# Optimization experiments

Hardware: AMD Instinct MI355X
Metric: run time of the kernel (lower is better)

## Reference

```python
import jax, jax.numpy as jnp
import numpy as np

DIM = 512
HEADS = 8
HEAD_DIM = 64
RS = 16        # region_size
EPEG_K = 15
L_TOKENS = 36864  # 192^2, multiple of RS^2 grid


def setup_inputs() -> dict:
    key = jax.random.key(0)
    ks = jax.random.split(key, 5)
    s = 1.0 / np.sqrt(DIM)
    x = jax.random.normal(ks[0], (1, L_TOKENS, DIM), jnp.float32)
    W_qkv = jax.random.normal(ks[1], (3 * HEADS * HEAD_DIM, DIM), jnp.float32) * s
    b_qkv = jnp.zeros((3 * HEADS * HEAD_DIM,), jnp.float32)
    W_proj = jax.random.normal(ks[2], (DIM, HEADS * HEAD_DIM), jnp.float32) * s
    b_proj = jnp.zeros((DIM,), jnp.float32)
    pe_w = jax.random.normal(ks[3], (HEADS, 1, EPEG_K, 1), jnp.float32) * 0.05
    pe_b = jnp.zeros((HEADS,), jnp.float32)
    return dict(x=x, W_qkv=W_qkv, b_qkv=b_qkv, W_proj=W_proj, b_proj=b_proj,
                pe_w=pe_w, pe_b=pe_b)


def reference(x, W_qkv, b_qkv, W_proj, b_proj, pe_w, pe_b):
    B, L, C = x.shape
    # --- padding() logic: square to HxW, H multiple of region_size ---
    H = int(np.ceil(np.sqrt(L)))
    H += (-H) % RS
    W = H
    add = H * W - L
    if add > 0:
        x = jnp.concatenate([x, jnp.zeros((B, add, C), x.dtype)], axis=1)
    # --- region_partition: (B,H,W,C) -> (num_regions*B, RS*RS, C) ---
    xr = (x.reshape(B, H // RS, RS, W // RS, RS, C)
            .transpose(0, 1, 3, 2, 4, 5)
            .reshape(-1, RS * RS, C))
    B_, N, _ = xr.shape
    # --- InnerAttention ---
    qkv = xr @ W_qkv.T + b_qkv                       # (B_, N, 3*h*d)
    qkv = qkv.reshape(B_, N, 3, HEADS, HEAD_DIM).transpose(2, 0, 3, 1, 4)
    q, k, v = qkv[0], qkv[1], qkv[2]                 # each (B_, h, N, d)
    scale = HEAD_DIM ** -0.5
    attn = jnp.einsum('bhid,bhjd->bhij', q * scale, k)   # (B_, h, N, N)
    # EPEG: depthwise conv (k,1) over the query axis of the score map
    pad = EPEG_K // 2
    pe = jax.lax.conv_general_dilated(
        attn, pe_w, window_strides=(1, 1), padding=((pad, pad), (0, 0)),
        dimension_numbers=('NCHW', 'OIHW', 'NCHW'), feature_group_count=HEADS)
    pe = pe + pe_b[None, :, None, None]
    attn = jax.nn.softmax(attn + pe, axis=-1)
    out = jnp.einsum('bhij,bhjd->bhid', attn, v)     # (B_, h, N, d)
    out = out.transpose(0, 2, 1, 3).reshape(B_, N, HEADS * HEAD_DIM)
    out = out @ W_proj.T + b_proj                    # (B_, N, C)
    # --- region_reverse ---
    out = (out.reshape(B, H // RS, W // RS, RS, RS, C)
              .transpose(0, 1, 3, 2, 4, 5)
              .reshape(B, H * W, C))
    if add > 0:
        out = out[:, :L]
    return out
```

## Files before the change

### kernel.cpp

```cpp
#include <hip/hip_runtime.h>
#include <stdint.h>

typedef __attribute__((ext_vector_type(8))) __bf16 bf16x8;
typedef __attribute__((ext_vector_type(16))) float f32x16;

__device__ __forceinline__ unsigned short f2bf(float f) {
  union { float f; unsigned int u; } v;
  v.f = f;
  unsigned int u = v.u;
  return (unsigned short)((u + 0x7FFFu + ((u >> 16) & 1u)) >> 16);
}

union BFrag { unsigned short u[8]; unsigned int w[4]; bf16x8 v; };

__device__ __forceinline__ f32x16 mfma32(bf16x8 a, bf16x8 b, f32x16 c) {
  return __builtin_amdgcn_mfma_f32_32x32x16_bf16(a, b, c, 0, 0, 0);
}

#define GLOAD_LDS16(gptr, lptr)                                                \
  __builtin_amdgcn_global_load_lds(                                           \
      (const __attribute__((address_space(1))) void*)(gptr),                  \
      (__attribute__((address_space(3))) void*)(lptr), 16, 0, 0)

__global__ __launch_bounds__(256) void k_xgather(const float* __restrict__ x,
                                                 unsigned short* __restrict__ xb) {
  int idx = blockIdx.x * 256 + threadIdx.x;
  int m = idx >> 6;
  int seg = (idx & 63) << 3;
  int r = m >> 8, n = m & 255;
  int a = r / 12, b = r - a * 12;
  int ii = n >> 4, jj = n & 15;
  long g = (long)((a * 16 + ii) * 192 + b * 16 + jj);
  const float4* p = (const float4*)(x + g * 512 + seg);
  float4 v0 = p[0], v1 = p[1];
  union { unsigned short u[8]; int4 v; } o;
  o.u[0] = f2bf(v0.x); o.u[1] = f2bf(v0.y); o.u[2] = f2bf(v0.z); o.u[3] = f2bf(v0.w);
  o.u[4] = f2bf(v1.x); o.u[5] = f2bf(v1.y); o.u[6] = f2bf(v1.z); o.u[7] = f2bf(v1.w);
  *(int4*)(xb + (size_t)m * 512 + seg) = o.v;
}

__global__ __launch_bounds__(256) void k_cvt(const float* __restrict__ s,
                                             unsigned short* __restrict__ d, int n8) {
  int i = blockIdx.x * 256 + threadIdx.x;
  if (i >= n8) return;
  const float4* p = (const float4*)(s + (size_t)i * 8);
  float4 a = p[0], b = p[1];
  union { unsigned short u[8]; int4 v; } o;
  o.u[0] = f2bf(a.x); o.u[1] = f2bf(a.y); o.u[2] = f2bf(a.z); o.u[3] = f2bf(a.w);
  o.u[4] = f2bf(b.x); o.u[5] = f2bf(b.y); o.u[6] = f2bf(b.z); o.u[7] = f2bf(b.w);
  *(int4*)(d + (size_t)i * 8) = o.v;
}

template<int MODE, int NBN>
__global__ __launch_bounds__(256, 2) void k_gemm(
    const unsigned short* __restrict__ A, const unsigned short* __restrict__ B,
    const float* __restrict__ bias,
    unsigned short* __restrict__ qb, unsigned short* __restrict__ kb,
    unsigned short* __restrict__ vtb, float* __restrict__ out) {
  __shared__ unsigned short As[8192];
  __shared__ unsigned short Bs[8192];
  int t = threadIdx.x;
  constexpr int NWG = NBN * 288;
  int d0 = blockIdx.x;
  int tl = (d0 & 7) * (NWG >> 3) + (d0 >> 3);
  int bm = tl / NBN, bn = tl % NBN;

  int w = t >> 6, lane = t & 63;
  int l31 = lane & 31, lh = lane >> 5;
  int wr = w >> 1, wc = w & 1;

  int srow = t >> 3, cseg = t & 7;
  int csw = (cseg ^ (srow & 7)) << 3;
  int ldsWaveOff = (t >> 6) << 10;

  f32x16 acc[2][2];
  for (int i = 0; i < 2; ++i)
    for (int j = 0; j < 2; ++j)
      for (int e = 0; e < 16; ++e) acc[i][j][e] = 0.0f;

  const unsigned short* Ag = A + (size_t)(bm * 128 + srow) * 512 + csw;
  const unsigned short* Bg = B + (size_t)(bn * 128 + srow) * 512 + csw;

  for (int ks = 0; ks < 8; ++ks) {
#pragma unroll
    for (int rnd = 0; rnd < 4; ++rnd) {
      GLOAD_LDS16(Ag + (size_t)rnd * 32 * 512 + ks * 64,
                  (char*)As + ldsWaveOff + rnd * 4096);
      GLOAD_LDS16(Bg + (size_t)rnd * 32 * 512 + ks * 64,
                  (char*)Bs + ldsWaveOff + rnd * 4096);
    }
    __syncthreads();
#pragma unroll
    for (int kt = 0; kt < 4; ++kt) {
      bf16x8 af[2], bfr[2];
#pragma unroll
      for (int mt = 0; mt < 2; ++mt) {
        int r = wr * 64 + mt * 32 + l31;
        af[mt] = *(const bf16x8*)((const char*)As + r * 128 +
                                  ((kt * 32 + lh * 16) ^ ((r & 7) << 4)));
      }
#pragma unroll
      for (int nt = 0; nt < 2; ++nt) {
        int r = wc * 64 + nt * 32 + l31;
        bfr[nt] = *(const bf16x8*)((const char*)Bs + r * 128 +
                                   ((kt * 32 + lh * 16) ^ ((r & 7) << 4)));
      }
#pragma unroll
      for (int mt = 0; mt < 2; ++mt)
#pragma unroll
        for (int nt = 0; nt < 2; ++nt)
          acc[mt][nt] = mfma32(af[mt], bfr[nt], acc[mt][nt]);
    }
    __syncthreads();
  }

  int nBase = bn * 128 + wc * 64;
  int mBase = bm * 128 + wr * 64;
#pragma unroll
  for (int nt = 0; nt < 2; ++nt) {
    int nn = nBase + nt * 32 + l31;
    float bs = bias[nn];
    if (MODE == 0) {
      int tsel = nn >> 9, rem = nn & 511;
      int hh = rem >> 6, d = rem & 63;
#pragma unroll
      for (int mt = 0; mt < 2; ++mt) {
#pragma unroll
        for (int q = 0; q < 4; ++q) {
          int m0 = mBase + mt * 32 + q * 8 + lh * 4;
          int r = m0 >> 8, tok = m0 & 255;
          size_t base = (size_t)(r * 8 + hh) * 16384;
          if (tsel == 0) {
#pragma unroll
            for (int j = 0; j < 4; ++j)
              qb[base + (size_t)(tok + j) * 64 + d] = f2bf((acc[mt][nt][q * 4 + j] + bs) * 0.125f);
          } else if (tsel == 1) {
#pragma unroll
            for (int j = 0; j < 4; ++j)
              kb[base + (size_t)(tok + j) * 64 + d] = f2bf(acc[mt][nt][q * 4 + j] + bs);
          } else {
            unsigned long long pv = 0;
#pragma unroll
            for (int j = 0; j < 4; ++j)
              pv |= (unsigned long long)f2bf(acc[mt][nt][q * 4 + j] + bs) << (16 * j);
            *(unsigned long long*)(vtb + base + (size_t)d * 256 + tok) = pv;
          }
        }
      }
    } else {
#pragma unroll
      for (int mt = 0; mt < 2; ++mt) {
#pragma unroll
        for (int q = 0; q < 4; ++q) {
          int m0 = mBase + mt * 32 + q * 8 + lh * 4;
          int r = m0 >> 8;
          int a = r / 12, bcol = r - a * 12;
#pragma unroll
          for (int j = 0; j < 4; ++j) {
            int tok = (m0 & 255) + j;
            int ii = tok >> 4, jj = tok & 15;
            long gg = (long)((a * 16 + ii) * 192 + bcol * 16 + jj);
            out[gg * 512 + nn] = acc[mt][nt][q * 4 + j] + bs;
          }
        }
      }
    }
  }
}

__global__ __launch_bounds__(512, 4) void k_attn6(
    const unsigned short* __restrict__ qb, const unsigned short* __restrict__ kb,
    const unsigned short* __restrict__ vtb, const float* __restrict__ pe_w,
    unsigned short* __restrict__ ctxb) {
  extern __shared__ char lds[];
  int rh = blockIdx.x;
  int h = rh & 7;
  int t = threadIdx.x, w = t >> 6, lane = t & 63;
  int l31 = lane & 31, lh = lane >> 5;
  int iw = w << 5;
  int myi = iw + l31;

  const unsigned short* Qg = qb + (size_t)rh * 16384;
  const unsigned short* Kg = kb + (size_t)rh * 16384;
  const unsigned short* Vg = vtb + (size_t)rh * 16384;
  const float* wh = pe_w + h * 15;

#pragma unroll
  for (int rr = 0; rr < 4; ++rr) {
    int row = rr * 64 + (t >> 3);
    GLOAD_LDS16(Kg + row * 64 + (((t & 7) ^ (row & 7)) << 3), lds + rr * 8192 + t * 16);
  }
  if (t < 96) {
    int dlo = t - 40, dhi = t - 39;
    unsigned int lo = (dlo >= 0 && dlo < 15) ? f2bf(wh[dlo]) : 0;
    unsigned int hi = (dhi >= 0 && dhi < 15) ? f2bf(wh[dhi]) : 0;
    *(unsigned int*)(lds + 57344 + t * 4) = lo | (hi << 16);
  }
  bf16x8 qf[4];
#pragma unroll
  for (int kt = 0; kt < 4; ++kt)
    qf[kt] = *(const bf16x8*)(Qg + (size_t)myi * 64 + kt * 16 + lh * 8);
  __syncthreads();

  float m = -3.0e38f, l = 0.0f;
  f32x16 acco[2];
#pragma unroll
  for (int nt = 0; nt < 2; ++nt)
#pragma unroll
    for (int e = 0; e < 16; ++e) acco[nt][e] = 0.0f;

#pragma unroll
  for (int it = 0; it < 8; ++it) {
    f32x16 sacc;
#pragma unroll
    for (int e = 0; e < 16; ++e) sacc[e] = 0.0f;
    {
      int kr = it * 32 + l31;
#pragma unroll
      for (int kt = 0; kt < 4; ++kt) {
        bf16x8 kf = *(const bf16x8*)(lds + kr * 128 + (((kt * 2 + lh) ^ (kr & 7)) << 4));
        sacc = mfma32(kf, qf[kt], sacc);
      }
    }
    __syncthreads();

    if ((it & 1) == 0) {
      int row = t >> 3;
      GLOAD_LDS16(Vg + row * 256 + it * 32 + (((t & 7) ^ (row & 7)) << 3),
                  lds + 49152 + t * 16);
    }

    {
      int i2 = myi * 2;
#pragma unroll
      for (int rg = 0; rg < 16; ++rg) {
        int jl = (rg & 3) + 8 * (rg >> 2) + 4 * lh;
        *(unsigned short*)(lds + 32768 + jl * 512 + (i2 ^ ((jl & 7) << 4))) =
            f2bf(sacc[rg]);
      }
    }
    __syncthreads();

    {
      int jl = l31;
#pragma unroll
      for (int u = 0; u < 4; ++u) {
        int ktg = 2 * w + u - 1;
        if (ktg >= 0 && ktg < 16) {
          BFrag bb;
          int d0 = 16 * u + 8 * lh - l31 + 31;
#pragma unroll
          for (int e2 = 0; e2 < 4; ++e2)
            bb.w[e2] = *(const unsigned int*)(lds + 57344 + (d0 + 2 * e2) * 4);
          bf16x8 sfr = *(const bf16x8*)(lds + 32768 + jl * 512 +
                                        ((ktg * 32 + lh * 16) ^ ((jl & 7) << 4)));
          sacc = mfma32(sfr, bb.v, sacc);
        }
      }
    }

    unsigned int pk[8];
    {
      float pm = -3.0e38f;
#pragma unroll
      for (int e = 0; e < 16; ++e) pm = fmaxf(pm, sacc[e]);
      pm = fmaxf(pm, __shfl_xor(pm, 32));
      float mn = fmaxf(m, pm);
      float f = __expf(m - mn);
      float ts = 0.0f;
#pragma unroll
      for (int u = 0; u < 8; ++u) {
        float p0 = __expf(sacc[2 * u] - mn);
        float p1 = __expf(sacc[2 * u + 1] - mn);
        ts += p0;
        ts += p1;
        pk[u] = (unsigned int)f2bf(p0) | ((unsigned int)f2bf(p1) << 16);
      }
      ts += __shfl_xor(ts, 32);
      l = (it == 0) ? ts : l * f + ts;
      m = mn;
      if (it != 0) {
#pragma unroll
        for (int rg = 0; rg < 16; ++rg) {
          float g = __shfl(f, (rg & 3) + 8 * (rg >> 2) + 4 * lh);
          acco[0][rg] *= g;
          acco[1][rg] *= g;
        }
      }
    }

    {
      unsigned int sw[8];
#pragma unroll
      for (int u = 0; u < 8; ++u) sw[u] = (unsigned int)__shfl_xor((int)pk[u], 32);
      BFrag pf0, pf1;
      if (lh == 0) {
        pf0.w[0] = pk[0]; pf0.w[1] = pk[1]; pf0.w[2] = sw[0]; pf0.w[3] = sw[1];
        pf1.w[0] = pk[4]; pf1.w[1] = pk[5]; pf1.w[2] = sw[4]; pf1.w[3] = sw[5];
      } else {
        pf0.w[0] = sw[2]; pf0.w[1] = sw[3]; pf0.w[2] = pk[2]; pf0.w[3] = pk[3];
        pf1.w[0] = sw[6]; pf1.w[1] = sw[7]; pf1.w[2] = pk[6]; pf1.w[3] = pk[7];
      }
      int kj0 = (it & 1) * 2;
#pragma unroll
      for (int nt = 0; nt < 2; ++nt) {
        int vr = nt * 32 + l31;
        bf16x8 vf0 = *(const bf16x8*)(lds + 49152 + vr * 128 +
                                      (((kj0 * 2 + lh) ^ (vr & 7)) << 4));
        bf16x8 vf1 = *(const bf16x8*)(lds + 49152 + vr * 128 +
                                      ((((kj0 + 1) * 2 + lh) ^ (vr & 7)) << 4));
        acco[nt] = mfma32(pf0.v, vf0, acco[nt]);
        acco[nt] = mfma32(pf1.v, vf1, acco[nt]);
      }
    }
  }

  float inv = 1.0f / l;
  int r256 = (rh >> 3) * 256;
  int chbase = h * 64;
#pragma unroll
  for (int rg = 0; rg < 16; ++rg) {
    int cr = (rg & 3) + 8 * (rg >> 2) + 4 * lh;
    float g = __shfl(inv, cr);
    int i = iw + cr;
    size_t rowoff = (size_t)(r256 + i) * 512 + chbase;
    ctxb[rowoff + l31] = f2bf(acco[0][rg] * g);
    ctxb[rowoff + 32 + l31] = f2bf(acco[1][rg] * g);
  }
}

extern "C" void kernel_launch(void* const* d_in, const int* in_sizes, int n_in,
                              void* d_out, int out_size, void* d_ws, size_t ws_size,
                              hipStream_t stream) {
  const float* x = (const float*)d_in[0];
  const float* Wqkv = (const float*)d_in[1];
  const float* bqkv = (const float*)d_in[2];
  const float* Wproj = (const float*)d_in[3];
  const float* bproj = (const float*)d_in[4];
  const float* pew = (const float*)d_in[5];

  char* ws = (char*)d_ws;
  unsigned short* xb = (unsigned short*)ws;
  unsigned short* wqkvb = (unsigned short*)(ws + 37748736);
  unsigned short* wprojb = (unsigned short*)(ws + 39321600);
  unsigned short* qb = (unsigned short*)(ws + 39845888);
  unsigned short* kb = (unsigned short*)(ws + 77594624);
  unsigned short* vtb = (unsigned short*)(ws + 115343360);

  (void)hipFuncSetAttribute((const void*)k_attn6,
                            hipFuncAttributeMaxDynamicSharedMemorySize, 163840);

  k_xgather<<<9216, 256, 0, stream>>>(x, xb);
  k_cvt<<<384, 256, 0, stream>>>(Wqkv, wqkvb, 98304);
  k_cvt<<<128, 256, 0, stream>>>(Wproj, wprojb, 32768);
  k_gemm<0, 12><<<3456, 256, 0, stream>>>(xb, wqkvb, bqkv, qb, kb, vtb, nullptr);
  k_attn6<<<1152, 512, 57728, stream>>>(qb, kb, vtb, pew, xb);
  k_gemm<1, 4><<<1152, 256, 0, stream>>>(xb, wprojb, bproj, nullptr, nullptr, nullptr,
                                         (float*)d_out);
}
```

Measured before the change: 244.7 us.

## Software-pipeline attention: double-buffer score tiles and V tiles, one barrier per step

Restructures the attention loop so the QK^T scores for the next key block are computed and staged into a second LDS buffer while the current block runs through the EPEG conv, softmax and PV. V tiles are also double-buffered and prefetched one step ahead, which cuts the loop from two barriers per iteration to one. The cost is more LDS (about 82KB per block, up from about 58KB) and extra accumulator registers. Launch bounds are relaxed from 4 to 2 blocks per SM, which lowers occupancy.

```diff
diff --git a/kernel.cpp b/kernel.cpp
--- a/kernel.cpp
+++ b/kernel.cpp
@@ -168,7 +168,7 @@
   }
 }
 
-__global__ __launch_bounds__(512, 4) void k_attn6(
+__global__ __launch_bounds__(512, 2) void k_attn7(
     const unsigned short* __restrict__ qb, const unsigned short* __restrict__ kb,
     const unsigned short* __restrict__ vtb, const float* __restrict__ pe_w,
     unsigned short* __restrict__ ctxb) {
@@ -190,11 +190,15 @@
     int row = rr * 64 + (t >> 3);
     GLOAD_LDS16(Kg + row * 64 + (((t & 7) ^ (row & 7)) << 3), lds + rr * 8192 + t * 16);
   }
+  {
+    int row = t >> 3;
+    GLOAD_LDS16(Vg + row * 256 + (((t & 7) ^ (row & 7)) << 3), lds + 65536 + t * 16);
+  }
   if (t < 96) {
     int dlo = t - 40, dhi = t - 39;
     unsigned int lo = (dlo >= 0 && dlo < 15) ? f2bf(wh[dlo]) : 0;
     unsigned int hi = (dhi >= 0 && dhi < 15) ? f2bf(wh[dhi]) : 0;
-    *(unsigned int*)(lds + 57344 + t * 4) = lo | (hi << 16);
+    *(unsigned int*)(lds + 81920 + t * 4) = lo | (hi << 16);
   }
   bf16x8 qf[4];
 #pragma unroll
@@ -209,37 +213,35 @@
 #pragma unroll
     for (int e = 0; e < 16; ++e) acco[nt][e] = 0.0f;
 
+  f32x16 sc[2];
+
+#pragma unroll
+  for (int e = 0; e < 16; ++e) sc[0][e] = 0.0f;
+  {
+    int kr = l31;
+#pragma unroll
+    for (int kt = 0; kt < 4; ++kt) {
+      bf16x8 kf = *(const bf16x8*)(lds + kr * 128 + (((kt * 2 + lh) ^ (kr & 7)) << 4));
+      sc[0] = mfma32(kf, qf[kt], sc[0]);
+    }
+  }
+  {
+    int i2 = myi * 2;
+#pragma unroll
+    for (int rg = 0; rg < 16; ++rg) {
+      int jl = (rg & 3) + 8 * (rg >> 2) + 4 * lh;
+      *(unsigned short*)(lds + 32768 + jl * 512 + (i2 ^ ((jl & 7) << 4))) =
+          f2bf(sc[0][rg]);
+    }
+  }
+  __syncthreads();
+
 #pragma unroll
   for (int it = 0; it < 8; ++it) {
-    f32x16 sacc;
-#pragma unroll
-    for (int e = 0; e < 16; ++e) sacc[e] = 0.0f;
-    {
-      int kr = it * 32 + l31;
-#pragma unroll
-      for (int kt = 0; kt < 4; ++kt) {
-        bf16x8 kf = *(const bf16x8*)(lds + kr * 128 + (((kt * 2 + lh) ^ (kr & 7)) << 4));
-        sacc = mfma32(kf, qf[kt], sacc);
-      }
-    }
-    __syncthreads();
-
-    if ((it & 1) == 0) {
-      int row = t >> 3;
-      GLOAD_LDS16(Vg + row * 256 + it * 32 + (((t & 7) ^ (row & 7)) << 3),
-                  lds + 49152 + t * 16);
-    }
-
-    {
-      int i2 = myi * 2;
-#pragma unroll
-      for (int rg = 0; rg < 16; ++rg) {
-        int jl = (rg & 3) + 8 * (rg >> 2) + 4 * lh;
-        *(unsigned short*)(lds + 32768 + jl * 512 + (i2 ^ ((jl & 7) << 4))) =
-            f2bf(sacc[rg]);
-      }
-    }
-    __syncthreads();
+    const int cur = it & 1, nxt = cur ^ 1;
+    char* sbuf = lds + 32768 + cur * 16384;
+    char* sbufN = lds + 32768 + nxt * 16384;
+    char* vbuf = lds + 65536 + ((it >> 1) & 1) * 8192;
 
     {
       int jl = l31;
@@ -251,11 +253,22 @@
           int d0 = 16 * u + 8 * lh - l31 + 31;
 #pragma unroll
           for (int e2 = 0; e2 < 4; ++e2)
-            bb.w[e2] = *(const unsigned int*)(lds + 57344 + (d0 + 2 * e2) * 4);
-          bf16x8 sfr = *(const bf16x8*)(lds + 32768 + jl * 512 +
+            bb.w[e2] = *(const unsigned int*)(lds + 81920 + (d0 + 2 * e2) * 4);
+          bf16x8 sfr = *(const bf16x8*)(sbuf + jl * 512 +
                                         ((ktg * 32 + lh * 16) ^ ((jl & 7) << 4)));
-          sacc = mfma32(sfr, bb.v, sacc);
+          sc[cur] = mfma32(sfr, bb.v, sc[cur]);
         }
+      }
+    }
+
+    if (it < 7) {
+#pragma unroll
+      for (int e = 0; e < 16; ++e) sc[nxt][e] = 0.0f;
+      int kr = (it + 1) * 32 + l31;
+#pragma unroll
+      for (int kt = 0; kt < 4; ++kt) {
+        bf16x8 kf = *(const bf16x8*)(lds + kr * 128 + (((kt * 2 + lh) ^ (kr & 7)) << 4));
+        sc[nxt] = mfma32(kf, qf[kt], sc[nxt]);
       }
     }
 
@@ -263,15 +276,15 @@
     {
       float pm = -3.0e38f;
 #pragma unroll
-      for (int e = 0; e < 16; ++e) pm = fmaxf(pm, sacc[e]);
+      for (int e = 0; e < 16; ++e) pm = fmaxf(pm, sc[cur][e]);
       pm = fmaxf(pm, __shfl_xor(pm, 32));
       float mn = fmaxf(m, pm);
       float f = __expf(m - mn);
       float ts = 0.0f;
 #pragma unroll
       for (int u = 0; u < 8; ++u) {
-        float p0 = __expf(sacc[2 * u] - mn);
-        float p1 = __expf(sacc[2 * u + 1] - mn);
+        float p0 = __expf(sc[cur][2 * u] - mn);
+        float p1 = __expf(sc[cur][2 * u + 1] - mn);
         ts += p0;
         ts += p1;
         pk[u] = (unsigned int)f2bf(p0) | ((unsigned int)f2bf(p1) << 16);
@@ -287,6 +300,23 @@
           acco[1][rg] *= g;
         }
       }
+    }
+
+    if (it < 7) {
+      int i2 = myi * 2;
+#pragma unroll
+      for (int rg = 0; rg < 16; ++rg) {
+        int jl = (rg & 3) + 8 * (rg >> 2) + 4 * lh;
+        *(unsigned short*)(sbufN + jl * 512 + (i2 ^ ((jl & 7) << 4))) =
+            f2bf(sc[nxt][rg]);
+      }
+    }
+
+    if ((it & 1) == 0 && it <= 4) {
+      int row = t >> 3;
+      int jb64 = (it / 2 + 1) * 64;
+      GLOAD_LDS16(Vg + row * 256 + jb64 + (((t & 7) ^ (row & 7)) << 3),
+                  lds + 65536 + (((it / 2 + 1) & 1) * 8192) + t * 16);
     }
 
     {
@@ -305,14 +335,16 @@
 #pragma unroll
       for (int nt = 0; nt < 2; ++nt) {
         int vr = nt * 32 + l31;
-        bf16x8 vf0 = *(const bf16x8*)(lds + 49152 + vr * 128 +
+        bf16x8 vf0 = *(const bf16x8*)(vbuf + vr * 128 +
                                       (((kj0 * 2 + lh) ^ (vr & 7)) << 4));
-        bf16x8 vf1 = *(const bf16x8*)(lds + 49152 + vr * 128 +
+        bf16x8 vf1 = *(const bf16x8*)(vbuf + vr * 128 +
                                       ((((kj0 + 1) * 2 + lh) ^ (vr & 7)) << 4));
         acco[nt] = mfma32(pf0.v, vf0, acco[nt]);
         acco[nt] = mfma32(pf1.v, vf1, acco[nt]);
       }
     }
+
+    __syncthreads();
   }
 
   float inv = 1.0f / l;
@@ -347,14 +379,14 @@
   unsigned short* kb = (unsigned short*)(ws + 77594624);
   unsigned short* vtb = (unsigned short*)(ws + 115343360);
 
-  (void)hipFuncSetAttribute((const void*)k_attn6,
+  (void)hipFuncSetAttribute((const void*)k_attn7,
                             hipFuncAttributeMaxDynamicSharedMemorySize, 163840);
 
   k_xgather<<<9216, 256, 0, stream>>>(x, xb);
   k_cvt<<<384, 256, 0, stream>>>(Wqkv, wqkvb, 98304);
   k_cvt<<<128, 256, 0, stream>>>(Wproj, wprojb, 32768);
   k_gemm<0, 12><<<3456, 256, 0, stream>>>(xb, wqkvb, bqkv, qb, kb, vtb, nullptr);
-  k_attn6<<<1152, 512, 57728, stream>>>(qb, kb, vtb, pew, xb);
+  k_attn7<<<1152, 512, 82304, stream>>>(qb, kb, vtb, pew, xb);
   k_gemm<1, 4><<<1152, 256, 0, stream>>>(xb, wprojb, bproj, nullptr, nullptr, nullptr,
                                          (float*)d_out);
 }
```

After: 227.3 us. -7.1%, faster.

## Split attention query rows across two blocks with halo recompute and K/V double buffering

Applied to the files above, without the earlier changes.

Each region-head is now processed by two 256-thread blocks, each handling 128 query rows. The 16-row conv halo at each side is recomputed by one rotating wave per key tile. K is no longer loaded whole up front: K and V tiles are streamed through double-buffered LDS, which shrinks LDS per block and may allow more blocks per CU. A block-index swizzle groups heads for L2 locality. The trade-off is duplicated halo QK work, more blocks, and extra prefetch logic.

```diff
diff --git a/kernel.cpp b/kernel.cpp
--- a/kernel.cpp
+++ b/kernel.cpp
@@ -168,38 +168,54 @@
   }
 }
 
-__global__ __launch_bounds__(512, 4) void k_attn6(
+__global__ __launch_bounds__(256, 3) void k_attn8(
     const unsigned short* __restrict__ qb, const unsigned short* __restrict__ kb,
     const unsigned short* __restrict__ vtb, const float* __restrict__ pe_w,
     unsigned short* __restrict__ ctxb) {
   extern __shared__ char lds[];
-  int rh = blockIdx.x;
+  int bid = blockIdx.x;
+  int tl = (bid & 7) * 288 + (bid >> 3);
+  int rh = tl >> 1;
+  int ibase = (tl & 1) << 7;
   int h = rh & 7;
   int t = threadIdx.x, w = t >> 6, lane = t & 63;
   int l31 = lane & 31, lh = lane >> 5;
-  int iw = w << 5;
-  int myi = iw + l31;
+  int myi = ibase + (w << 5) + l31;
 
   const unsigned short* Qg = qb + (size_t)rh * 16384;
   const unsigned short* Kg = kb + (size_t)rh * 16384;
   const unsigned short* Vg = vtb + (size_t)rh * 16384;
   const float* wh = pe_w + h * 15;
 
-#pragma unroll
-  for (int rr = 0; rr < 4; ++rr) {
-    int row = rr * 64 + (t >> 3);
-    GLOAD_LDS16(Kg + row * 64 + (((t & 7) ^ (row & 7)) << 3), lds + rr * 8192 + t * 16);
+  {
+    int row = t >> 3;
+    GLOAD_LDS16(Kg + row * 64 + (((t & 7) ^ (row & 7)) << 3), lds + t * 16);
+#pragma unroll
+    for (int rr = 0; rr < 2; ++rr) {
+      int vrow = rr * 32 + row;
+      GLOAD_LDS16(Vg + vrow * 256 + (((t & 7) ^ (vrow & 7)) << 3),
+                  lds + 8192 + rr * 4096 + t * 16);
+    }
   }
   if (t < 96) {
     int dlo = t - 40, dhi = t - 39;
     unsigned int lo = (dlo >= 0 && dlo < 15) ? f2bf(wh[dlo]) : 0;
     unsigned int hi = (dhi >= 0 && dhi < 15) ? f2bf(wh[dhi]) : 0;
-    *(unsigned int*)(lds + 57344 + t * 4) = lo | (hi << 16);
-  }
-  bf16x8 qf[4];
-#pragma unroll
-  for (int kt = 0; kt < 4; ++kt)
-    qf[kt] = *(const bf16x8*)(Qg + (size_t)myi * 64 + kt * 16 + lh * 8);
+    *(unsigned int*)(lds + 36864 + t * 4) = lo | (hi << 16);
+  }
+  bf16x8 qf[4], qh[4];
+  {
+    int ihl = ibase + ((l31 < 16) ? (l31 - 16) : (112 + l31));
+    bool hok = (ihl >= 0) && (ihl < 256);
+    int ihc = hok ? ihl : 0;
+    BFrag zf; zf.w[0] = zf.w[1] = zf.w[2] = zf.w[3] = 0;
+#pragma unroll
+    for (int kt = 0; kt < 4; ++kt) {
+      qf[kt] = *(const bf16x8*)(Qg + (size_t)myi * 64 + kt * 16 + lh * 8);
+      bf16x8 qv = *(const bf16x8*)(Qg + (size_t)ihc * 64 + kt * 16 + lh * 8);
+      qh[kt] = hok ? qv : zf.v;
+    }
+  }
   __syncthreads();
 
   float m = -3.0e38f, l = 0.0f;
@@ -211,31 +227,62 @@
 
 #pragma unroll
   for (int it = 0; it < 8; ++it) {
+    char* kbuf = lds + (it & 1) * 4096;
+    char* vbuf = lds + 8192 + ((it >> 1) & 1) * 8192;
+
     f32x16 sacc;
 #pragma unroll
     for (int e = 0; e < 16; ++e) sacc[e] = 0.0f;
     {
-      int kr = it * 32 + l31;
+      int kr = l31;
 #pragma unroll
       for (int kt = 0; kt < 4; ++kt) {
-        bf16x8 kf = *(const bf16x8*)(lds + kr * 128 + (((kt * 2 + lh) ^ (kr & 7)) << 4));
+        bf16x8 kf = *(const bf16x8*)(kbuf + kr * 128 + (((kt * 2 + lh) ^ (kr & 7)) << 4));
         sacc = mfma32(kf, qf[kt], sacc);
       }
     }
     __syncthreads();
 
-    if ((it & 1) == 0) {
+    if (it < 7) {
       int row = t >> 3;
-      GLOAD_LDS16(Vg + row * 256 + it * 32 + (((t & 7) ^ (row & 7)) << 3),
-                  lds + 49152 + t * 16);
-    }
-
-    {
-      int i2 = myi * 2;
+      GLOAD_LDS16(Kg + (32 * (it + 1) + row) * 64 + (((t & 7) ^ (row & 7)) << 3),
+                  lds + ((it + 1) & 1) * 4096 + t * 16);
+    }
+    if ((it & 1) && it < 7) {
+      int row = t >> 3;
+      int jb = 32 * (it + 1);
+#pragma unroll
+      for (int rr = 0; rr < 2; ++rr) {
+        int vrow = rr * 32 + row;
+        GLOAD_LDS16(Vg + vrow * 256 + jb + (((t & 7) ^ (vrow & 7)) << 3),
+                    lds + 8192 + (((it + 1) >> 1) & 1) * 8192 + rr * 4096 + t * 16);
+      }
+    }
+
+    if (w == (it & 3)) {
+      f32x16 sh;
+#pragma unroll
+      for (int e = 0; e < 16; ++e) sh[e] = 0.0f;
+      int kr = l31;
+#pragma unroll
+      for (int kt = 0; kt < 4; ++kt) {
+        bf16x8 kf = *(const bf16x8*)(kbuf + kr * 128 + (((kt * 2 + lh) ^ (kr & 7)) << 4));
+        sh = mfma32(kf, qh[kt], sh);
+      }
+      int cH2 = ((l31 < 16) ? l31 : (128 + l31)) * 2;
 #pragma unroll
       for (int rg = 0; rg < 16; ++rg) {
         int jl = (rg & 3) + 8 * (rg >> 2) + 4 * lh;
-        *(unsigned short*)(lds + 32768 + jl * 512 + (i2 ^ ((jl & 7) << 4))) =
+        *(unsigned short*)(lds + 24576 + jl * 384 + (cH2 ^ ((jl & 7) << 4))) =
+            f2bf(sh[rg]);
+      }
+    }
+    {
+      int cM2 = (16 + (w << 5) + l31) * 2;
+#pragma unroll
+      for (int rg = 0; rg < 16; ++rg) {
+        int jl = (rg & 3) + 8 * (rg >> 2) + 4 * lh;
+        *(unsigned short*)(lds + 24576 + jl * 384 + (cM2 ^ ((jl & 7) << 4))) =
             f2bf(sacc[rg]);
       }
     }
@@ -245,17 +292,15 @@
       int jl = l31;
 #pragma unroll
       for (int u = 0; u < 4; ++u) {
-        int ktg = 2 * w + u - 1;
-        if (ktg >= 0 && ktg < 16) {
-          BFrag bb;
-          int d0 = 16 * u + 8 * lh - l31 + 31;
-#pragma unroll
-          for (int e2 = 0; e2 < 4; ++e2)
-            bb.w[e2] = *(const unsigned int*)(lds + 57344 + (d0 + 2 * e2) * 4);
-          bf16x8 sfr = *(const bf16x8*)(lds + 32768 + jl * 512 +
-                                        ((ktg * 32 + lh * 16) ^ ((jl & 7) << 4)));
-          sacc = mfma32(sfr, bb.v, sacc);
-        }
+        int k = 2 * w + u;
+        BFrag bb;
+        int d0 = 16 * u + 8 * lh - l31 + 31;
+#pragma unroll
+        for (int e2 = 0; e2 < 4; ++e2)
+          bb.w[e2] = *(const unsigned int*)(lds + 36864 + (d0 + 2 * e2) * 4);
+        bf16x8 sfr = *(const bf16x8*)(lds + 24576 + jl * 384 +
+                                      ((k * 32 + lh * 16) ^ ((jl & 7) << 4)));
+        sacc = mfma32(sfr, bb.v, sacc);
       }
     }
 
@@ -305,9 +350,9 @@
 #pragma unroll
       for (int nt = 0; nt < 2; ++nt) {
         int vr = nt * 32 + l31;
-        bf16x8 vf0 = *(const bf16x8*)(lds + 49152 + vr * 128 +
+        bf16x8 vf0 = *(const bf16x8*)(vbuf + vr * 128 +
                                       (((kj0 * 2 + lh) ^ (vr & 7)) << 4));
-        bf16x8 vf1 = *(const bf16x8*)(lds + 49152 + vr * 128 +
+        bf16x8 vf1 = *(const bf16x8*)(vbuf + vr * 128 +
                                       ((((kj0 + 1) * 2 + lh) ^ (vr & 7)) << 4));
         acco[nt] = mfma32(pf0.v, vf0, acco[nt]);
         acco[nt] = mfma32(pf1.v, vf1, acco[nt]);
@@ -322,7 +367,7 @@
   for (int rg = 0; rg < 16; ++rg) {
     int cr = (rg & 3) + 8 * (rg >> 2) + 4 * lh;
     float g = __shfl(inv, cr);
-    int i = iw + cr;
+    int i = ibase + (w << 5) + cr;
     size_t rowoff = (size_t)(r256 + i) * 512 + chbase;
     ctxb[rowoff + l31] = f2bf(acco[0][rg] * g);
     ctxb[rowoff + 32 + l31] = f2bf(acco[1][rg] * g);
@@ -347,14 +392,14 @@
   unsigned short* kb = (unsigned short*)(ws + 77594624);
   unsigned short* vtb = (unsigned short*)(ws + 115343360);
 
-  (void)hipFuncSetAttribute((const void*)k_attn6,
+  (void)hipFuncSetAttribute((const void*)k_attn8,
                             hipFuncAttributeMaxDynamicSharedMemorySize, 163840);
 
   k_xgather<<<9216, 256, 0, stream>>>(x, xb);
   k_cvt<<<384, 256, 0, stream>>>(Wqkv, wqkvb, 98304);
   k_cvt<<<128, 256, 0, stream>>>(Wproj, wprojb, 32768);
   k_gemm<0, 12><<<3456, 256, 0, stream>>>(xb, wqkvb, bqkv, qb, kb, vtb, nullptr);
-  k_attn6<<<1152, 512, 57728, stream>>>(qb, kb, vtb, pew, xb);
+  k_attn8<<<2304, 256, 37248, stream>>>(qb, kb, vtb, pew, xb);
   k_gemm<1, 4><<<1152, 256, 0, stream>>>(xb, wprojb, bproj, nullptr, nullptr, nullptr,
                                          (float*)d_out);
 }
```

Result: slower. 315.4 us (+28.9%).

## Compute halo query scores per wave to remove block barriers in EPEG attention

Applied to the files above, without the earlier changes.

Each wave now recomputes the 16-row query halo scores on its own (extra MFMAs against neighbouring Q rows) and stages them in a private LDS tile. This removes the two block-wide __syncthreads per iteration that were needed to share score tiles across waves for the depthwise conv. The full V tile is preloaded into LDS up front instead of being streamed per iteration. In exchange it doubles the QK MFMA work, raises LDS use to about 100KB, and lowers the occupancy hint from 4 to 2 blocks.

```diff
diff --git a/kernel.cpp b/kernel.cpp
--- a/kernel.cpp
+++ b/kernel.cpp
@@ -168,7 +168,7 @@
   }
 }
 
-__global__ __launch_bounds__(512, 4) void k_attn6(
+__global__ __launch_bounds__(512, 2) void k_attn11(
     const unsigned short* __restrict__ qb, const unsigned short* __restrict__ kb,
     const unsigned short* __restrict__ vtb, const float* __restrict__ pe_w,
     unsigned short* __restrict__ ctxb) {
@@ -190,17 +190,35 @@
     int row = rr * 64 + (t >> 3);
     GLOAD_LDS16(Kg + row * 64 + (((t & 7) ^ (row & 7)) << 3), lds + rr * 8192 + t * 16);
   }
+#pragma unroll
+  for (int rr = 0; rr < 4; ++rr) {
+    int row = rr * 16 + (t >> 5);
+    int seg = t & 31;
+    int sseg = (seg & ~7) | ((seg & 7) ^ (row & 7));
+    GLOAD_LDS16(Vg + row * 256 + sseg * 8, lds + 32768 + rr * 8192 + t * 16);
+  }
   if (t < 96) {
     int dlo = t - 40, dhi = t - 39;
     unsigned int lo = (dlo >= 0 && dlo < 15) ? f2bf(wh[dlo]) : 0;
     unsigned int hi = (dhi >= 0 && dhi < 15) ? f2bf(wh[dhi]) : 0;
-    *(unsigned int*)(lds + 57344 + t * 4) = lo | (hi << 16);
-  }
-  bf16x8 qf[4];
-#pragma unroll
-  for (int kt = 0; kt < 4; ++kt)
-    qf[kt] = *(const bf16x8*)(Qg + (size_t)myi * 64 + kt * 16 + lh * 8);
+    *(unsigned int*)(lds + 100352 + t * 4) = lo | (hi << 16);
+  }
+  bf16x8 qf[4], qh[4];
+  {
+    int ihl = iw + ((l31 < 16) ? (l31 - 16) : (l31 + 16));
+    bool hok = (ihl >= 0) && (ihl < 256);
+    int ihc = hok ? ihl : 0;
+    BFrag zf; zf.w[0] = zf.w[1] = zf.w[2] = zf.w[3] = 0;
+#pragma unroll
+    for (int kt = 0; kt < 4; ++kt) {
+      qf[kt] = *(const bf16x8*)(Qg + (size_t)myi * 64 + kt * 16 + lh * 8);
+      bf16x8 qv = *(const bf16x8*)(Qg + (size_t)ihc * 64 + kt * 16 + lh * 8);
+      qh[kt] = hok ? qv : zf.v;
+    }
+  }
   __syncthreads();
+
+  char* st = lds + 65536 + w * 4352;
 
   float m = -3.0e38f, l = 0.0f;
   f32x16 acco[2];
@@ -211,52 +229,39 @@
 
 #pragma unroll
   for (int it = 0; it < 8; ++it) {
-    f32x16 sacc;
-#pragma unroll
-    for (int e = 0; e < 16; ++e) sacc[e] = 0.0f;
+    f32x16 sacc, sh;
+#pragma unroll
+    for (int e = 0; e < 16; ++e) { sacc[e] = 0.0f; sh[e] = 0.0f; }
     {
       int kr = it * 32 + l31;
 #pragma unroll
       for (int kt = 0; kt < 4; ++kt) {
         bf16x8 kf = *(const bf16x8*)(lds + kr * 128 + (((kt * 2 + lh) ^ (kr & 7)) << 4));
         sacc = mfma32(kf, qf[kt], sacc);
-      }
-    }
-    __syncthreads();
-
-    if ((it & 1) == 0) {
-      int row = t >> 3;
-      GLOAD_LDS16(Vg + row * 256 + it * 32 + (((t & 7) ^ (row & 7)) << 3),
-                  lds + 49152 + t * 16);
+        sh = mfma32(kf, qh[kt], sh);
+      }
     }
 
     {
-      int i2 = myi * 2;
+      int cO = (l31 + 16) * 2;
+      int cH = ((l31 < 16) ? l31 : (l31 + 32)) * 2;
 #pragma unroll
       for (int rg = 0; rg < 16; ++rg) {
-        int jl = (rg & 3) + 8 * (rg >> 2) + 4 * lh;
-        *(unsigned short*)(lds + 32768 + jl * 512 + (i2 ^ ((jl & 7) << 4))) =
-            f2bf(sacc[rg]);
-      }
-    }
-    __syncthreads();
-
-    {
-      int jl = l31;
-#pragma unroll
-      for (int u = 0; u < 4; ++u) {
-        int ktg = 2 * w + u - 1;
-        if (ktg >= 0 && ktg < 16) {
-          BFrag bb;
-          int d0 = 16 * u + 8 * lh - l31 + 31;
-#pragma unroll
-          for (int e2 = 0; e2 < 4; ++e2)
-            bb.w[e2] = *(const unsigned int*)(lds + 57344 + (d0 + 2 * e2) * 4);
-          bf16x8 sfr = *(const bf16x8*)(lds + 32768 + jl * 512 +
-                                        ((ktg * 32 + lh * 16) ^ ((jl & 7) << 4)));
-          sacc = mfma32(sfr, bb.v, sacc);
-        }
-      }
+        int j = (rg & 3) + 8 * (rg >> 2) + 4 * lh;
+        *(unsigned short*)(st + j * 136 + cO) = f2bf(sacc[rg]);
+        *(unsigned short*)(st + j * 136 + cH) = f2bf(sh[rg]);
+      }
+    }
+
+#pragma unroll
+    for (int u = 0; u < 4; ++u) {
+      BFrag bb;
+      int d0 = 16 * u + 8 * lh - l31 + 31;
+#pragma unroll
+      for (int e2 = 0; e2 < 4; ++e2)
+        bb.w[e2] = *(const unsigned int*)(lds + 100352 + (d0 + 2 * e2) * 4);
+      bf16x8 sfr = *(const bf16x8*)(st + l31 * 136 + (u * 16 + lh * 8) * 2);
+      sacc = mfma32(sfr, bb.v, sacc);
     }
 
     unsigned int pk[8];
@@ -301,14 +306,15 @@
         pf0.w[0] = sw[2]; pf0.w[1] = sw[3]; pf0.w[2] = pk[2]; pf0.w[3] = pk[3];
         pf1.w[0] = sw[6]; pf1.w[1] = sw[7]; pf1.w[2] = pk[6]; pf1.w[3] = pk[7];
       }
-      int kj0 = (it & 1) * 2;
 #pragma unroll
       for (int nt = 0; nt < 2; ++nt) {
         int vr = nt * 32 + l31;
-        bf16x8 vf0 = *(const bf16x8*)(lds + 49152 + vr * 128 +
-                                      (((kj0 * 2 + lh) ^ (vr & 7)) << 4));
-        bf16x8 vf1 = *(const bf16x8*)(lds + 49152 + vr * 128 +
-                                      ((((kj0 + 1) * 2 + lh) ^ (vr & 7)) << 4));
+        int c0 = it * 4 + lh;
+        int c1 = it * 4 + 2 + lh;
+        int c0s = (c0 & ~7) | ((c0 & 7) ^ (vr & 7));
+        int c1s = (c1 & ~7) | ((c1 & 7) ^ (vr & 7));
+        bf16x8 vf0 = *(const bf16x8*)(lds + 32768 + vr * 512 + c0s * 16);
+        bf16x8 vf1 = *(const bf16x8*)(lds + 32768 + vr * 512 + c1s * 16);
         acco[nt] = mfma32(pf0.v, vf0, acco[nt]);
         acco[nt] = mfma32(pf1.v, vf1, acco[nt]);
       }
@@ -347,14 +353,14 @@
   unsigned short* kb = (unsigned short*)(ws + 77594624);
   unsigned short* vtb = (unsigned short*)(ws + 115343360);
 
-  (void)hipFuncSetAttribute((const void*)k_attn6,
+  (void)hipFuncSetAttribute((const void*)k_attn11,
                             hipFuncAttributeMaxDynamicSharedMemorySize, 163840);
 
   k_xgather<<<9216, 256, 0, stream>>>(x, xb);
   k_cvt<<<384, 256, 0, stream>>>(Wqkv, wqkvb, 98304);
   k_cvt<<<128, 256, 0, stream>>>(Wproj, wprojb, 32768);
   k_gemm<0, 12><<<3456, 256, 0, stream>>>(xb, wqkvb, bqkv, qb, kb, vtb, nullptr);
-  k_attn6<<<1152, 512, 57728, stream>>>(qb, kb, vtb, pew, xb);
+  k_attn11<<<1152, 512, 100736, stream>>>(qb, kb, vtb, pew, xb);
   k_gemm<1, 4><<<1152, 256, 0, stream>>>(xb, wprojb, bproj, nullptr, nullptr, nullptr,
                                          (float*)d_out);
 }
```

Result: slower. 267.8 us (+9.4%).
